# Optimization experiments

Measured on AMD Instinct MI355X. Metric: run time of the kernel, lower is better.

The kernel has to match this reference:

```python
import jax, jax.numpy as jnp
import numpy as np

B, DIM = 16, 256          # batch, grid size
K, NKER = 7, 15           # FD stencil size, total FD kernels for max_order=4 (orders 00..hk, incl. D00)
STEPS = 32                # stepnum
DT = 0.5                  # self.dt
MU = 1.0                  # permeability constant (original: vacuum permeability)
FREQ = 0.05               # source frequency
PAD = (K - 1) // 2
CX = CY = DIM // 2        # point-source location


def setup_inputs() -> dict:
    key = jax.random.key(0)
    k1, k2, k3, k4, k5, k6 = jax.random.split(key, 6)
    u1 = jax.random.normal(k1, (B, 1, DIM, DIM), jnp.float32) * 0.01
    u0 = jax.random.normal(k2, (B, 1, DIM, DIM), jnp.float32) * 0.01
    epsr = jax.random.uniform(k3, (B, 1, DIM, DIM), jnp.float32) + 1.0   # permittivity >= 1
    sigma = jax.random.uniform(k4, (B, 1, DIM, DIM), jnp.float32)        # conductivity
    fd_kernels = jax.random.normal(k5, (NKER, 1, K, K), jnp.float32) * 0.01  # FD2d moment-bank stencils
    combo_w = jax.random.normal(k6, (1, NKER - 1, 1, 1), jnp.float32) * 1e-3  # combofd 1x1 conv weight
    # j_gen source: jj0_i = Re((1+c)^i) * delta, jj2_i = Re((1+c)^(i+2)) * delta, c = dt*2*pi*f*(-1+1j)
    c = DT * 2.0 * np.pi * FREQ * (-1.0 + 1.0j)
    p = (1.0 + c) ** np.arange(STEPS + 2)
    src = jnp.asarray(np.stack([p[2:STEPS + 2].real, p[:STEPS].real], axis=1), jnp.float32)  # [STEPS, 2]=(jj2, jj0)
    return {"u1": u1, "u0": u0, "epsr": epsr, "sigma": sigma,
            "fd_kernels": fd_kernels, "combo_w": combo_w, "src": src, "stepnum": STEPS}


def _fdtd(u1, u0, epsr, sigma, fd_kernels, combo_w, src):
    dt = jnp.float32(DT)
    mu = jnp.float32(MU)
    inv_den = 1.0 / (2.0 * epsr / dt + sigma)       # 1/(2*epsr/dt + sigma)
    a = 4.0 * epsr / dt                             # coeff of u1id
    b = 2.0 * epsr / dt - sigma                     # coeff of u0id
    cw = combo_w[:, :, 0, 0]                        # [1, NKER-1] (1x1 conv)

    def step(carry, s):
        u0c, u1c = carry
        # FD stencil bank: [B,1,H,W] -> [B,NKER,H,W], zero (Dirichlet) padding
        u1fd = jax.lax.conv_general_dilated(
            u1c, fd_kernels, (1, 1), [(PAD, PAD), (PAD, PAD)],
            dimension_numbers=("NCHW", "OIHW", "NCHW"))
        # combofd: 1x1 conv over derivative channels (drop D00 identity channel)
        combo = jnp.einsum("bchw,oc->bohw", u1fd[:, 1:], cw)
        # id_u1/id_u0 are order-0 moment-constrained 1x1 kernels == identity
        rhs = (2.0 * dt / mu) * combo + a * u1c - b * u0c
        rhs = rhs.at[:, :, CX, CY].add(-(s[0] - s[1]))  # -(jj2 - jj0) point source
        u2 = inv_den * rhs
        return (u1c, u2), None

    (_, u2), _ = jax.lax.scan(step, (u0, u1), src)
    return u2


def reference(u1, u0, epsr, sigma, fd_kernels, combo_w, src, stepnum):
    return _fdtd(u1, u0, epsr, sigma, fd_kernels, combo_w, src)
```

## Files before the change

kernel.cpp:

```cpp
#include <hip/hip_runtime.h>

#define DIM   256
#define BATCH 16
#define NPX   (DIM*DIM)

#define PR   280
#define PC   284
#define PBS  (PR*PC)
#define NPAD ((size_t)BATCH*PBS)

#define LR 90
#define LC 100
#define CR 84

__global__ void prep_eff(const float* __restrict__ fdk,
                         const float* __restrict__ cw,
                         float* __restrict__ eff) {
    int t = threadIdx.x;
    if (t < 49) {
        float s = 0.f;
        #pragma unroll
        for (int c = 1; c < 15; ++c)
            s += fdk[c * 49 + t] * cw[c - 1];
        eff[t] = s;
    }
}

__global__ __launch_bounds__(1024) void prologue(
    const float* __restrict__ u1, const float* __restrict__ u0,
    const float* __restrict__ epsr, const float* __restrict__ sigma,
    float* __restrict__ A1, float* __restrict__ A0,
    float* __restrict__ B1, float* __restrict__ B0,
    float* __restrict__ CDp, float* __restrict__ CGp)
{
    const int i = blockIdx.x;
    const int b = 2 * (i & 7) + ((i >> 3) & 1);
    const int slice = i >> 4;
    const size_t gb = (size_t)b * NPX;
    const int start = slice * 7455, end = start + 7455;

    for (int w = start + (int)threadIdx.x; w < end; w += 1024) {
        const int kind = w / 19880;
        const int cell = w - kind * 19880;
        const int row = cell / 71, c4 = (cell - row * 71) * 4;
        const int gy = row - 12;
        float4 v = make_float4(0.f, 0.f, 0.f, 0.f);
        if (kind < 2) {
            const float* sp = kind ? u0 : u1;
            if (gy >= 0 && gy < DIM) {
                #pragma unroll
                for (int k = 0; k < 4; ++k) {
                    const int gx = c4 + k - 12;
                    if (gx >= 0 && gx < DIM)
                        ((float*)&v)[k] = sp[gb + gy * DIM + gx];
                }
            }
        } else if (kind >= 4) {
            if (gy >= 0 && gy < DIM) {
                #pragma unroll
                for (int k = 0; k < 4; ++k) {
                    const int gx = c4 + k - 12;
                    if (gx >= 0 && gx < DIM) {
                        const float e = epsr[gb + gy * DIM + gx];
                        const float s = sigma[gb + gy * DIM + gx];
                        const float d = 1.f / (4.f * e + s);
                        ((float*)&v)[k] = (kind == 4) ? d : (4.f * e - s) * d;
                    }
                }
            }
        }
        float* dst = (kind == 0) ? A1 : (kind == 1) ? A0 : (kind == 2) ? B1
                   : (kind == 3) ? B0 : (kind == 4) ? CDp : CGp;
        *(float4*)&dst[(size_t)b * PBS + (size_t)row * PC + c4] = v;
    }
}

template<int NB, int NG, int J0, int OFF>
__device__ __forceinline__ void substep(
    const float (*__restrict__ Fs)[LC], float (*__restrict__ Fd)[LC],
    const float (*__restrict__ CD)[LC], const float (*__restrict__ CG)[LC],
    const float* __restrict__ eff, float ds, bool srcHere, int t)
{
    constexpr int SLOTS = NB * NG;
    if (t < SLOTS) {
        const int band = t / NG;
        const int j    = J0 + (t - band * NG);
        const int pcol = 4 * j;
        const int yb   = OFF + 4 * band;

        float a[4][4] = {{0,0,0,0},{0,0,0,0},{0,0,0,0},{0,0,0,0}};
        #pragma unroll
        for (int ky = 0; ky < 10; ++ky) {
            const int row = yb - 3 + ky;
            const float4 q0 = *(const float4*)&Fs[row][pcol - 4];
            const float4 q1 = *(const float4*)&Fs[row][pcol];
            const float4 q2 = *(const float4*)&Fs[row][pcol + 4];
            const float v[12] = {q0.x,q0.y,q0.z,q0.w, q1.x,q1.y,q1.z,q1.w,
                                 q2.x,q2.y,q2.z,q2.w};
            #pragma unroll
            for (int o = 0; o < 4; ++o) {
                const int kh = ky - o;
                if (kh >= 0 && kh < 7) {
                    #pragma unroll
                    for (int kx = 0; kx < 7; ++kx) {
                        const float E = eff[kh * 7 + kx];
                        a[o][0] = fmaf(v[kx + 1], E, a[o][0]);
                        a[o][1] = fmaf(v[kx + 2], E, a[o][1]);
                        a[o][2] = fmaf(v[kx + 3], E, a[o][2]);
                        a[o][3] = fmaf(v[kx + 4], E, a[o][3]);
                    }
                }
            }
        }
        #pragma unroll
        for (int o = 0; o < 4; ++o) {
            const int row = yb + o;
            const float4 u1q = *(const float4*)&Fs[row][pcol];
            const float4 u0q = *(const float4*)&Fd[row][pcol];
            const float4 dq  = *(const float4*)&CD[row - 3][pcol];
            const float4 gq  = *(const float4*)&CG[row - 3][pcol];
            float4 r;
            r.x = fmaf(dq.x, a[o][0], fmaf(gq.x, u1q.x - u0q.x, u1q.x));
            r.y = fmaf(dq.y, a[o][1], fmaf(gq.y, u1q.y - u0q.y, u1q.y));
            r.z = fmaf(dq.z, a[o][2], fmaf(gq.z, u1q.z - u0q.z, u1q.z));
            r.w = fmaf(dq.w, a[o][3], fmaf(gq.w, u1q.w - u0q.w, u1q.w));
            if (srcHere && row == 12 && pcol == 16)
                r.x = fmaf(-dq.x, ds, r.x);
            *(float4*)&Fd[row][pcol] = r;
        }
    }
}

__global__ __launch_bounds__(1024) void fdtd4(
    const float* __restrict__ U1, const float* __restrict__ U0,
    const float* __restrict__ CDg, const float* __restrict__ CGg,
    const float* __restrict__ eff, const float* __restrict__ src,
    float* __restrict__ NU1, int n1bs, int n1rs, int n1off,
    float* __restrict__ NU0, int sbase)
{
    __shared__ __align__(16) float F[2][LR][LC];
    __shared__ __align__(16) float CD[CR][LC];
    __shared__ __align__(16) float CG[CR][LC];

    const int t = threadIdx.x;
    const int i = blockIdx.x;
    const int b    = 2 * (i & 7) + ((i >> 3) & 1);
    const int tile = i >> 4;
    const int bx = tile & 3, by = tile >> 2;
    const bool srcHere = (bx == 2 && by == 2);
    const size_t pbF = (size_t)b * PBS;

    {
        const float* s1 = U1 + pbF;
        const float* s0 = U0 + pbF;
        const float* sd = CDg + pbF;
        const float* sg = CGg + pbF;
        #pragma unroll
        for (int rep = 0; rep < 4; ++rep) {
            const int idx = t + rep * 1024;
            if (idx < 2 * 1936) {
                const int arr = idx >= 1936 ? 1 : 0;
                const int j2  = idx - arr * 1936;
                const int row = j2 / 22, c4 = (j2 - row * 22) * 4;
                const float4 v = *(const float4*)
                    &(arr ? s0 : s1)[(size_t)(by * 64 + row) * PC + bx * 64 + c4];
                *(float4*)&F[arr][row][4 + c4] = v;
            }
        }
        #pragma unroll
        for (int rep = 0; rep < 4; ++rep) {
            const int idx = t + rep * 1024;
            if (idx < 2 * 1848) {
                const int arr = idx >= 1848 ? 1 : 0;
                const int j2  = idx - arr * 1848;
                const int row = j2 / 22, c4 = (j2 - row * 22) * 4;
                const float4 v = *(const float4*)
                    &(arr ? sg : sd)[(size_t)(by * 64 + 3 + row) * PC + bx * 64 + c4];
                if (arr) *(float4*)&CG[row][4 + c4] = v;
                else     *(float4*)&CD[row][4 + c4] = v;
            }
        }
    }
    __syncthreads();

    const float ds0 = src[2 * sbase]     - src[2 * sbase + 1];
    const float ds1 = src[2 * sbase + 2] - src[2 * sbase + 3];
    const float ds2 = src[2 * sbase + 4] - src[2 * sbase + 5];
    const float ds3 = src[2 * sbase + 6] - src[2 * sbase + 7];

    substep<21, 22, 1,  3>(F[0], F[1], CD, CG, eff, ds0, srcHere, t); __syncthreads();
    substep<19, 20, 2,  6>(F[1], F[0], CD, CG, eff, ds1, srcHere, t); __syncthreads();
    substep<18, 18, 3,  9>(F[0], F[1], CD, CG, eff, ds2, srcHere, t); __syncthreads();
    substep<16, 16, 4, 12>(F[1], F[0], CD, CG, eff, ds3, srcHere, t); __syncthreads();

    {
        const int row = t >> 4, c = (t & 15) * 4;
        const int gy = by * 64 + row, gx = bx * 64 + c;
        const float4 o1 = *(const float4*)&F[0][12 + row][16 + c];
        const float4 o0 = *(const float4*)&F[1][12 + row][16 + c];
        *(float4*)&NU1[(size_t)b * n1bs + (size_t)(gy + n1off) * n1rs + gx + n1off] = o1;
        *(float4*)&NU0[pbF + (size_t)(gy + 12) * PC + gx + 12] = o0;
    }
}

extern "C" void kernel_launch(void* const* d_in, const int* in_sizes, int n_in,
                              void* d_out, int out_size, void* d_ws, size_t ws_size,
                              hipStream_t stream) {
    (void)in_sizes; (void)n_in; (void)out_size; (void)ws_size;

    const float* u1    = (const float*)d_in[0];
    const float* u0    = (const float*)d_in[1];
    const float* epsr  = (const float*)d_in[2];
    const float* sigma = (const float*)d_in[3];
    const float* fdk   = (const float*)d_in[4];
    const float* cw    = (const float*)d_in[5];
    const float* src   = (const float*)d_in[6];

    float* eff = (float*)d_ws;
    float* A1  = eff + 64;
    float* A0  = A1 + NPAD;
    float* B1  = A0 + NPAD;
    float* B0  = B1 + NPAD;
    float* CDg = B0 + NPAD;
    float* CGg = CDg + NPAD;

    prep_eff<<<1, 64, 0, stream>>>(fdk, cw, eff);
    prologue<<<256, 1024, 0, stream>>>(u1, u0, epsr, sigma, A1, A0, B1, B0, CDg, CGg);

    for (int j = 0; j < 8; ++j) {
        const float* cu1 = (j & 1) ? B1 : A1;
        const float* cu0 = (j & 1) ? B0 : A0;
        float* n1 = (j & 1) ? A1 : B1;
        float* n0 = (j & 1) ? A0 : B0;
        int bs = PBS, rs = PC, off = 12;
        if (j == 7) { n1 = (float*)d_out; bs = NPX; rs = DIM; off = 0; }
        fdtd4<<<256, 1024, 0, stream>>>(cu1, cu0, CDg, CGg, eff, src,
                                        n1, bs, rs, off, n0, 4 * j);
    }
}
```

Baseline: 248.1 us.

## Halve tile height and read coefficient fields directly from global memory

Spatial tiles shrink from 64x64 to 32x64 output rows, doubling the grid to 512 blocks. The CD/CG coefficient arrays are no longer staged in shared memory and are read from global memory in the update epilogue. This cuts shared memory per block, which may let more blocks run per CU and fills the GPU better. The cost is more redundant halo recomputation per output from the smaller tiles, and uncached global reads of the coefficients in each substep.

```diff
diff --git a/kernel.cpp b/kernel.cpp
--- a/kernel.cpp
+++ b/kernel.cpp
@@ -9,9 +9,8 @@
 #define PBS  (PR*PC)
 #define NPAD ((size_t)BATCH*PBS)
 
-#define LR 90
+#define LR 58
 #define LC 100
-#define CR 84
 
 __global__ void prep_eff(const float* __restrict__ fdk,
                          const float* __restrict__ cw,
@@ -78,7 +77,7 @@
 template<int NB, int NG, int J0, int OFF>
 __device__ __forceinline__ void substep(
     const float (*__restrict__ Fs)[LC], float (*__restrict__ Fd)[LC],
-    const float (*__restrict__ CD)[LC], const float (*__restrict__ CG)[LC],
+    const float* __restrict__ CDb, const float* __restrict__ CGb,
     const float* __restrict__ eff, float ds, bool srcHere, int t)
 {
     constexpr int SLOTS = NB * NG;
@@ -115,10 +114,10 @@
         #pragma unroll
         for (int o = 0; o < 4; ++o) {
             const int row = yb + o;
+            const float4 dq  = *(const float4*)&CDb[row * PC + pcol];
+            const float4 gq  = *(const float4*)&CGb[row * PC + pcol];
             const float4 u1q = *(const float4*)&Fs[row][pcol];
             const float4 u0q = *(const float4*)&Fd[row][pcol];
-            const float4 dq  = *(const float4*)&CD[row - 3][pcol];
-            const float4 gq  = *(const float4*)&CG[row - 3][pcol];
             float4 r;
             r.x = fmaf(dq.x, a[o][0], fmaf(gq.x, u1q.x - u0q.x, u1q.x));
             r.y = fmaf(dq.y, a[o][1], fmaf(gq.y, u1q.y - u0q.y, u1q.y));
@@ -139,63 +138,50 @@
     float* __restrict__ NU0, int sbase)
 {
     __shared__ __align__(16) float F[2][LR][LC];
-    __shared__ __align__(16) float CD[CR][LC];
-    __shared__ __align__(16) float CG[CR][LC];
 
     const int t = threadIdx.x;
     const int i = blockIdx.x;
     const int b    = 2 * (i & 7) + ((i >> 3) & 1);
     const int tile = i >> 4;
-    const int bx = tile & 3, by = tile >> 2;
-    const bool srcHere = (bx == 2 && by == 2);
+    const int bx = tile & 3, ty = tile >> 2;
+    const bool srcHere = (bx == 2 && ty == 4);
     const size_t pbF = (size_t)b * PBS;
+    const size_t tofs = (size_t)(ty * 32) * PC + bx * 64;
 
     {
-        const float* s1 = U1 + pbF;
-        const float* s0 = U0 + pbF;
-        const float* sd = CDg + pbF;
-        const float* sg = CGg + pbF;
-        #pragma unroll
-        for (int rep = 0; rep < 4; ++rep) {
+        const float* s1 = U1 + pbF + tofs;
+        const float* s0 = U0 + pbF + tofs;
+        #pragma unroll
+        for (int rep = 0; rep < 3; ++rep) {
             const int idx = t + rep * 1024;
-            if (idx < 2 * 1936) {
-                const int arr = idx >= 1936 ? 1 : 0;
-                const int j2  = idx - arr * 1936;
+            if (idx < 2 * 1232) {
+                const int arr = idx >= 1232 ? 1 : 0;
+                const int j2  = idx - arr * 1232;
                 const int row = j2 / 22, c4 = (j2 - row * 22) * 4;
                 const float4 v = *(const float4*)
-                    &(arr ? s0 : s1)[(size_t)(by * 64 + row) * PC + bx * 64 + c4];
+                    &(arr ? s0 : s1)[(size_t)row * PC + c4];
                 *(float4*)&F[arr][row][4 + c4] = v;
             }
         }
-        #pragma unroll
-        for (int rep = 0; rep < 4; ++rep) {
-            const int idx = t + rep * 1024;
-            if (idx < 2 * 1848) {
-                const int arr = idx >= 1848 ? 1 : 0;
-                const int j2  = idx - arr * 1848;
-                const int row = j2 / 22, c4 = (j2 - row * 22) * 4;
-                const float4 v = *(const float4*)
-                    &(arr ? sg : sd)[(size_t)(by * 64 + 3 + row) * PC + bx * 64 + c4];
-                if (arr) *(float4*)&CG[row][4 + c4] = v;
-                else     *(float4*)&CD[row][4 + c4] = v;
-            }
-        }
     }
     __syncthreads();
+
+    const float* CDb = CDg + pbF + tofs - 4;
+    const float* CGb = CGg + pbF + tofs - 4;
 
     const float ds0 = src[2 * sbase]     - src[2 * sbase + 1];
     const float ds1 = src[2 * sbase + 2] - src[2 * sbase + 3];
     const float ds2 = src[2 * sbase + 4] - src[2 * sbase + 5];
     const float ds3 = src[2 * sbase + 6] - src[2 * sbase + 7];
 
-    substep<21, 22, 1,  3>(F[0], F[1], CD, CG, eff, ds0, srcHere, t); __syncthreads();
-    substep<19, 20, 2,  6>(F[1], F[0], CD, CG, eff, ds1, srcHere, t); __syncthreads();
-    substep<18, 18, 3,  9>(F[0], F[1], CD, CG, eff, ds2, srcHere, t); __syncthreads();
-    substep<16, 16, 4, 12>(F[1], F[0], CD, CG, eff, ds3, srcHere, t); __syncthreads();
-
-    {
+    substep<13, 22, 1,  3>(F[0], F[1], CDb, CGb, eff, ds0, srcHere, t); __syncthreads();
+    substep<11, 20, 2,  6>(F[1], F[0], CDb, CGb, eff, ds1, srcHere, t); __syncthreads();
+    substep<10, 18, 3,  9>(F[0], F[1], CDb, CGb, eff, ds2, srcHere, t); __syncthreads();
+    substep< 8, 16, 4, 12>(F[1], F[0], CDb, CGb, eff, ds3, srcHere, t); __syncthreads();
+
+    if (t < 512) {
         const int row = t >> 4, c = (t & 15) * 4;
-        const int gy = by * 64 + row, gx = bx * 64 + c;
+        const int gy = ty * 32 + row, gx = bx * 64 + c;
         const float4 o1 = *(const float4*)&F[0][12 + row][16 + c];
         const float4 o0 = *(const float4*)&F[1][12 + row][16 + c];
         *(float4*)&NU1[(size_t)b * n1bs + (size_t)(gy + n1off) * n1rs + gx + n1off] = o1;
@@ -234,7 +220,7 @@
         float* n0 = (j & 1) ? A0 : B0;
         int bs = PBS, rs = PC, off = 12;
         if (j == 7) { n1 = (float*)d_out; bs = NPX; rs = DIM; off = 0; }
-        fdtd4<<<256, 1024, 0, stream>>>(cu1, cu0, CDg, CGg, eff, src,
+        fdtd4<<<512, 1024, 0, stream>>>(cu1, cu0, CDg, CGg, eff, src,
                                         n1, bs, rs, off, n0, 4 * j);
     }
 }
```

Measured after the change: 288.2 us. 1.16x slower.
